# Optimization experiments

Hardware: AMD Instinct MI355X
Metric: run time of the kernel (lower is better)

The kernel has to match this reference:

```python
import jax, jax.numpy as jnp
import numpy as np

NEG_INF = -1e9  # masked_fill value in torch code
HELP_THRESH = -1e8  # help_scores > -1e8 marks valid dependency entries


def setup_inputs() -> dict:
    key = jax.random.key(0)
    ks = jax.random.split(key, 16)
    B, S, D, H, DK = 8, 512, 1024, 16, 64
    sc = 0.02
    x = jax.random.normal(ks[0], (B, S, D), jnp.float32)
    Wq = jax.random.normal(ks[1], (D, H * DK), jnp.float32) * sc
    bq = jax.random.normal(ks[2], (H * DK,), jnp.float32) * sc
    Wk = jax.random.normal(ks[3], (D, H * DK), jnp.float32) * sc
    bk = jax.random.normal(ks[4], (H * DK,), jnp.float32) * sc
    Wv = jax.random.normal(ks[5], (D, H * DK), jnp.float32) * sc
    bv = jax.random.normal(ks[6], (H * DK,), jnp.float32) * sc
    Wo = jax.random.normal(ks[7], (H * DK, D), jnp.float32) * sc
    bo = jax.random.normal(ks[8], (D,), jnp.float32) * sc
    ln_g = jnp.ones((D,), jnp.float32)
    ln_b = jnp.zeros((D,), jnp.float32)
    help_vals = jax.random.normal(ks[9], (B, H, S, S), jnp.float32)
    help_mask = jax.random.randint(ks[10], (B, H, S, S), 0, 2).astype(jnp.int32)
    attn_mask = jax.random.randint(ks[11], (B, S, S), 0, 2).astype(bool)
    return {"x": x, "Wq": Wq, "bq": bq, "Wk": Wk, "bk": bk, "Wv": Wv,
            "bv": bv, "Wo": Wo, "bo": bo, "ln_g": ln_g, "ln_b": ln_b,
            "help_vals": help_vals, "help_mask": help_mask, "attn_mask": attn_mask}


def reference(x, Wq, bq, Wk, bk, Wv, bv, Wo, bo, ln_g, ln_b,
              help_vals, help_mask, attn_mask):
    B, S, D = x.shape
    H, DK = 16, 64
    # projections -> [B,H,S,dk]
    q = (x @ Wq + bq).reshape(B, S, H, DK).transpose(0, 2, 1, 3)
    k = (x @ Wk + bk).reshape(B, S, H, DK).transpose(0, 2, 1, 3)
    v = (x @ Wv + bv).reshape(B, S, H, DK).transpose(0, 2, 1, 3)
    scores = jnp.einsum('bhqd,bhkd->bhqk', q, k) / np.sqrt(DK).astype(np.float32)
    scores = jnp.where(attn_mask[:, None, :, :], NEG_INF, scores)
    # dependency-tree score blending (ScaledDotProductAttention)
    help_scores = jnp.where(help_mask.astype(bool), help_vals, NEG_INF)
    m = (help_scores > HELP_THRESH).astype(scores.dtype)
    dep_w = m * 0.5
    seq_w = m * 0.5 + (1.0 - m)
    scores = help_scores * dep_w + scores * seq_w
    attn = jax.nn.softmax(scores, axis=-1)
    ctx = jnp.einsum('bhqk,bhkd->bhqd', attn, v)  # [B,H,S,dv]
    ctx = ctx.transpose(0, 2, 1, 3).reshape(B, S, H * DK)
    out = ctx @ Wo + bo
    # residual + LayerNorm (input_dim == output_dim path)
    y = out + x
    mu = y.mean(-1, keepdims=True)
    var = ((y - mu) ** 2).mean(-1, keepdims=True)
    y = (y - mu) / jnp.sqrt(var + 1e-5) * ln_g + ln_b
    return y, attn
```

## Files before the change

### kernel.cpp

```cpp
#include <hip/hip_runtime.h>
#include <hip/hip_bf16.h>

typedef __bf16 bf16_t;
typedef __bf16 bf16x4 __attribute__((ext_vector_type(4)));
typedef __bf16 bf16x8 __attribute__((ext_vector_type(8)));
typedef float f32x4 __attribute__((ext_vector_type(4)));
typedef int i32x4 __attribute__((ext_vector_type(4)));


__device__ __forceinline__ f32x4 mfma16(bf16x8 a, bf16x8 b, f32x4 c) {
    return __builtin_amdgcn_mfma_f32_16x16x32_bf16(a, b, c, 0, 0, 0);
}

__device__ __forceinline__ float blendf(float s, int am, int hm, float hv) {
    s = am ? -1e9f : s;
    return hm ? 0.5f * hv + 0.5f * s : s;
}

#define GLOAD_LDS16(g, l)                                                   \
    __builtin_amdgcn_global_load_lds(                                       \
        (const __attribute__((address_space(1))) void*)(g),                 \
        (__attribute__((address_space(3))) void*)(l), 16, 0, 0)

__global__ __launch_bounds__(256) void cast_kernel(const float* __restrict__ x,
                                                   bf16_t* __restrict__ xb) {
    size_t i = ((size_t)blockIdx.x * 256 + threadIdx.x) * 4;
    float4 v = *(const float4*)(x + i);
    bf16x4 o;
    o[0] = (bf16_t)v.x; o[1] = (bf16_t)v.y; o[2] = (bf16_t)v.z; o[3] = (bf16_t)v.w;
    *(bf16x4*)(xb + i) = o;
}

__global__ __launch_bounds__(256) void transpose_kernel(const float* __restrict__ Wq,
                                                        const float* __restrict__ Wk,
                                                        const float* __restrict__ Wv,
                                                        const float* __restrict__ Wo,
                                                        bf16_t* __restrict__ Wt_base) {
    __shared__ float tile[32][33];
    const int z = blockIdx.z;
    const float* W = (z == 0) ? Wq : (z == 1) ? Wk : (z == 2) ? Wv : Wo;
    bf16_t* Wt = Wt_base + ((size_t)z << 20);
    int tx = threadIdx.x & 31, ty = threadIdx.x >> 5;
    int bx = blockIdx.x * 32, by = blockIdx.y * 32;
#pragma unroll
    for (int j = 0; j < 4; j++)
        tile[ty + j * 8][tx] = W[(size_t)(by + ty + j * 8) * 1024 + bx + tx];
    __syncthreads();
#pragma unroll
    for (int j = 0; j < 4; j++)
        Wt[(size_t)(bx + ty + j * 8) * 1024 + by + tx] = (bf16_t)tile[tx][ty + j * 8];
}

__global__ __launch_bounds__(256, 4) void gemm_qkv(const bf16_t* __restrict__ A,
                                                   const bf16_t* __restrict__ WtB,
                                                   const float* __restrict__ bq,
                                                   const float* __restrict__ bk,
                                                   const float* __restrict__ bv,
                                                   bf16_t* __restrict__ qb,
                                                   bf16_t* __restrict__ kb,
                                                   bf16_t* __restrict__ vt) {
    constexpr int K = 1024;
    __shared__ bf16_t As[2][128][32];
    __shared__ bf16_t Bs[2][128][32];
    const int z = blockIdx.z;
    const bf16_t* Bt = WtB + ((size_t)z << 20);
    const float* bias = (z == 0) ? bq : (z == 1) ? bk : bv;
    const int t = threadIdx.x;
    const int lane = t & 63, wv = t >> 6;
    const int lm = lane & 15, q4 = lane >> 4;
    const int mblk = blockIdx.y * 128, nblk = blockIdx.x * 128;
    const int mrow = (wv & 1) * 64, ncol = (wv >> 1) * 64;
    const int sr = t >> 2, sc = (t & 3) * 8;

    f32x4 acc[4][4];
#pragma unroll
    for (int r = 0; r < 4; r++)
#pragma unroll
        for (int c = 0; c < 4; c++) acc[r][c] = (f32x4){0.f, 0.f, 0.f, 0.f};

    const bf16_t* ga = &A[(size_t)(mblk + sr) * K + sc];
    const bf16_t* gb = &Bt[(size_t)(nblk + sr) * K + sc];
    GLOAD_LDS16(ga, &As[0][sr][sc]);
    GLOAD_LDS16(ga + (size_t)64 * K, &As[0][sr + 64][sc]);
    GLOAD_LDS16(gb, &Bs[0][sr][sc]);
    GLOAD_LDS16(gb + (size_t)64 * K, &Bs[0][sr + 64][sc]);
    __syncthreads();

    int cur = 0;
    for (int k0 = 0; k0 < K; k0 += 32) {
        if (k0 + 32 < K) {
            const bf16_t* ga2 = ga + k0 + 32;
            const bf16_t* gb2 = gb + k0 + 32;
            GLOAD_LDS16(ga2, &As[cur ^ 1][sr][sc]);
            GLOAD_LDS16(ga2 + (size_t)64 * K, &As[cur ^ 1][sr + 64][sc]);
            GLOAD_LDS16(gb2, &Bs[cur ^ 1][sr][sc]);
            GLOAD_LDS16(gb2 + (size_t)64 * K, &Bs[cur ^ 1][sr + 64][sc]);
        }
        bf16x8 af[4], bfr[4];
#pragma unroll
        for (int r = 0; r < 4; r++) af[r] = *(const bf16x8*)&As[cur][mrow + r * 16 + lm][q4 * 8];
#pragma unroll
        for (int c = 0; c < 4; c++) bfr[c] = *(const bf16x8*)&Bs[cur][ncol + c * 16 + lm][q4 * 8];
#pragma unroll
        for (int r = 0; r < 4; r++)
#pragma unroll
            for (int c = 0; c < 4; c++) acc[r][c] = mfma16(af[r], bfr[c], acc[r][c]);
        __syncthreads();
        cur ^= 1;
    }

#pragma unroll
    for (int r = 0; r < 4; r++)
#pragma unroll
        for (int c = 0; c < 4; c++)
#pragma unroll
            for (int i = 0; i < 4; i++) {
                int m = mblk + mrow + r * 16 + q4 * 4 + i;
                int n = nblk + ncol + c * 16 + lm;
                float v = acc[r][c][i] + bias[n];
                int b = m >> 9, s = m & 511, h = n >> 6, d = n & 63;
                if (z < 2) {
                    bf16_t* o = z ? kb : qb;
                    o[(((size_t)(b * 16 + h) * 512) + s) * 64 + d] = (bf16_t)v;
                } else {
                    vt[(((size_t)(b * 16 + h) * 64) + d) * 512 + s] = (bf16_t)v;
                }
            }
}

__global__ __launch_bounds__(256, 4) void gemm_out(const bf16_t* __restrict__ A,
                                                   const bf16_t* __restrict__ Bt,
                                                   const float* __restrict__ bias,
                                                   const float* __restrict__ resid,
                                                   float* __restrict__ outp) {
    constexpr int K = 1024, N = 1024;
    __shared__ bf16_t As[2][128][32];
    __shared__ bf16_t Bs[2][128][32];
    const int t = threadIdx.x;
    const int lane = t & 63, wv = t >> 6;
    const int lm = lane & 15, q4 = lane >> 4;
    const int mblk = blockIdx.y * 128, nblk = blockIdx.x * 128;
    const int mrow = (wv & 1) * 64, ncol = (wv >> 1) * 64;
    const int sr = t >> 2, sc = (t & 3) * 8;

    f32x4 acc[4][4];
#pragma unroll
    for (int r = 0; r < 4; r++)
#pragma unroll
        for (int c = 0; c < 4; c++) acc[r][c] = (f32x4){0.f, 0.f, 0.f, 0.f};

    const bf16_t* ga = &A[(size_t)(mblk + sr) * K + sc];
    const bf16_t* gb = &Bt[(size_t)(nblk + sr) * K + sc];
    GLOAD_LDS16(ga, &As[0][sr][sc]);
    GLOAD_LDS16(ga + (size_t)64 * K, &As[0][sr + 64][sc]);
    GLOAD_LDS16(gb, &Bs[0][sr][sc]);
    GLOAD_LDS16(gb + (size_t)64 * K, &Bs[0][sr + 64][sc]);
    __syncthreads();

    int cur = 0;
    for (int k0 = 0; k0 < K; k0 += 32) {
        if (k0 + 32 < K) {
            const bf16_t* ga2 = ga + k0 + 32;
            const bf16_t* gb2 = gb + k0 + 32;
            GLOAD_LDS16(ga2, &As[cur ^ 1][sr][sc]);
            GLOAD_LDS16(ga2 + (size_t)64 * K, &As[cur ^ 1][sr + 64][sc]);
            GLOAD_LDS16(gb2, &Bs[cur ^ 1][sr][sc]);
            GLOAD_LDS16(gb2 + (size_t)64 * K, &Bs[cur ^ 1][sr + 64][sc]);
        }
        bf16x8 af[4], bfr[4];
#pragma unroll
        for (int r = 0; r < 4; r++) af[r] = *(const bf16x8*)&As[cur][mrow + r * 16 + lm][q4 * 8];
#pragma unroll
        for (int c = 0; c < 4; c++) bfr[c] = *(const bf16x8*)&Bs[cur][ncol + c * 16 + lm][q4 * 8];
#pragma unroll
        for (int r = 0; r < 4; r++)
#pragma unroll
            for (int c = 0; c < 4; c++) acc[r][c] = mfma16(af[r], bfr[c], acc[r][c]);
        __syncthreads();
        cur ^= 1;
    }

#pragma unroll
    for (int r = 0; r < 4; r++)
#pragma unroll
        for (int c = 0; c < 4; c++)
#pragma unroll
            for (int i = 0; i < 4; i++) {
                int m = mblk + mrow + r * 16 + q4 * 4 + i;
                int n = nblk + ncol + c * 16 + lm;
                float v = acc[r][c][i] + bias[n];
                outp[(size_t)m * N + n] = v + resid[(size_t)m * N + n];
            }
}

__global__ __launch_bounds__(512, 8) void attn_fused_kernel(const bf16_t* __restrict__ Qb,
                                                            const bf16_t* __restrict__ Kb,
                                                            const bf16_t* __restrict__ Vt,
                                                            const float* __restrict__ help_vals,
                                                            const int* __restrict__ help_mask,
                                                            const int* __restrict__ attn_mask,
                                                            float* __restrict__ attn_out,
                                                            bf16_t* __restrict__ xo) {
    constexpr int SS = 516;
    const int t = threadIdx.x;
    const int lane = t & 63, wv = t >> 6;
    const int lm = lane & 15, q4 = lane >> 4;
    const int bh = blockIdx.y;
    const int b = bh >> 4, h = bh & 15;
    const int q0 = blockIdx.x * 16;
    const bf16_t* Qp = Qb + (size_t)bh * 512 * 64;
    const bf16_t* Kp = Kb + (size_t)bh * 512 * 64;
    const bf16_t* Vp = Vt + (size_t)bh * 64 * 512;

    __shared__ float S[16][SS];
    __shared__ float ctx[16][68];

    for (int i = t; i < 16 * 68; i += 512) ((float*)ctx)[i] = 0.f;

    const bf16x8 bq0 = *(const bf16x8*)&Qp[(size_t)(q0 + lm) * 64 + q4 * 8];
    const bf16x8 bq1 = *(const bf16x8*)&Qp[(size_t)(q0 + lm) * 64 + 32 + q4 * 8];
    f32x4 acc[4];
#pragma unroll
    for (int j = 0; j < 4; j++) acc[j] = (f32x4){0.f, 0.f, 0.f, 0.f};
    __builtin_amdgcn_s_setprio(1);
#pragma unroll
    for (int j = 0; j < 4; j++) {
        const int krow = wv * 64 + j * 16 + lm;
        bf16x8 ak0 = *(const bf16x8*)&Kp[(size_t)krow * 64 + q4 * 8];
        bf16x8 ak1 = *(const bf16x8*)&Kp[(size_t)krow * 64 + 32 + q4 * 8];
        acc[j] = mfma16(ak0, bq0, acc[j]);
        acc[j] = mfma16(ak1, bq1, acc[j]);
    }
    __builtin_amdgcn_s_setprio(0);
#pragma unroll
    for (int j = 0; j < 4; j++)
        *(f32x4*)&S[lm][wv * 64 + j * 16 + q4 * 4] = acc[j] * 0.125f;

    const int c0 = lane * 4, c1 = 256 + lane * 4;
    const int rbase = wv * 2;
    const size_t qrow0 = ((size_t)bh * 512 + q0 + rbase) * 512;
    const size_t arow0 = ((size_t)b * 512 + q0 + rbase) * 512;
    f32x4 hv[2][2];
    i32x4 hm[2][2], am[2][2];
#pragma unroll
    for (int rr = 0; rr < 2; rr++) {
        const size_t qr = qrow0 + (size_t)rr * 512;
        const size_t ar = arow0 + (size_t)rr * 512;
        hv[rr][0] = __builtin_nontemporal_load((const f32x4*)&help_vals[qr + c0]);
        hv[rr][1] = __builtin_nontemporal_load((const f32x4*)&help_vals[qr + c1]);
        hm[rr][0] = __builtin_nontemporal_load((const i32x4*)&help_mask[qr + c0]);
        hm[rr][1] = __builtin_nontemporal_load((const i32x4*)&help_mask[qr + c1]);
        am[rr][0] = *(const i32x4*)&attn_mask[ar + c0];
        am[rr][1] = *(const i32x4*)&attn_mask[ar + c1];
    }
    __builtin_amdgcn_sched_barrier(0);
    __syncthreads();

#pragma unroll
    for (int rr = 0; rr < 2; rr++) {
        const int r = rbase + rr;
        const size_t qrow = qrow0 + (size_t)rr * 512;
        f32x4 s0 = *(const f32x4*)&S[r][c0];
        f32x4 s1 = *(const f32x4*)&S[r][c1];
        float sv[8];
#pragma unroll
        for (int i = 0; i < 4; i++) sv[i] = blendf(s0[i], am[rr][0][i], hm[rr][0][i], hv[rr][0][i]);
#pragma unroll
        for (int i = 0; i < 4; i++)
            sv[4 + i] = blendf(s1[i], am[rr][1][i], hm[rr][1][i], hv[rr][1][i]);
        float mloc = fmaxf(fmaxf(fmaxf(sv[0], sv[1]), fmaxf(sv[2], sv[3])),
                           fmaxf(fmaxf(sv[4], sv[5]), fmaxf(sv[6], sv[7])));
#pragma unroll
        for (int off = 1; off < 64; off <<= 1) mloc = fmaxf(mloc, __shfl_xor(mloc, off));
        float lsum = 0.f;
#pragma unroll
        for (int i = 0; i < 8; i++) {
            sv[i] = __expf(sv[i] - mloc);
            lsum += sv[i];
        }
#pragma unroll
        for (int off = 1; off < 64; off <<= 1) lsum += __shfl_xor(lsum, off);
        const float rinv = 1.0f / lsum;
        f32x4 o0, o1;
        o0[0] = sv[0] * rinv; o0[1] = sv[1] * rinv; o0[2] = sv[2] * rinv; o0[3] = sv[3] * rinv;
        o1[0] = sv[4] * rinv; o1[1] = sv[5] * rinv; o1[2] = sv[6] * rinv; o1[3] = sv[7] * rinv;
        *(f32x4*)&S[r][c0] = o0;
        *(f32x4*)&S[r][c1] = o1;
        __builtin_nontemporal_store(o0, (f32x4*)&attn_out[qrow + c0]);
        __builtin_nontemporal_store(o1, (f32x4*)&attn_out[qrow + c1]);
    }
    __syncthreads();

    f32x4 acc2[4];
#pragma unroll
    for (int mt = 0; mt < 4; mt++) acc2[mt] = (f32x4){0.f, 0.f, 0.f, 0.f};
    const int kb0 = wv * 64;
    __builtin_amdgcn_s_setprio(1);
#pragma unroll
    for (int C = 0; C < 2; C++) {
        f32x4 pa = *(const f32x4*)&S[lm][kb0 + C * 32 + q4 * 8];
        f32x4 pb = *(const f32x4*)&S[lm][kb0 + C * 32 + q4 * 8 + 4];
        bf16x8 pf;
        pf[0] = (bf16_t)pa[0]; pf[1] = (bf16_t)pa[1]; pf[2] = (bf16_t)pa[2]; pf[3] = (bf16_t)pa[3];
        pf[4] = (bf16_t)pb[0]; pf[5] = (bf16_t)pb[1]; pf[6] = (bf16_t)pb[2]; pf[7] = (bf16_t)pb[3];
#pragma unroll
        for (int mt = 0; mt < 4; mt++) {
            const bf16x8 vf =
                *(const bf16x8*)&Vp[(size_t)(mt * 16 + lm) * 512 + kb0 + C * 32 + q4 * 8];
            acc2[mt] = mfma16(vf, pf, acc2[mt]);
        }
    }
    __builtin_amdgcn_s_setprio(0);
#pragma unroll
    for (int mt = 0; mt < 4; mt++)
#pragma unroll
        for (int i = 0; i < 4; i++) atomicAdd(&ctx[lm][mt * 16 + q4 * 4 + i], acc2[mt][i]);
    __syncthreads();

    if (t < 256) {
        const int qq = t >> 4;
        const int d4 = (t & 15) * 4;
        f32x4 sum = *(const f32x4*)&ctx[qq][d4];
        bf16x4 o;
        o[0] = (bf16_t)sum[0]; o[1] = (bf16_t)sum[1];
        o[2] = (bf16_t)sum[2]; o[3] = (bf16_t)sum[3];
        *(bf16x4*)&xo[((size_t)(b * 512 + q0 + qq)) * 1024 + h * 64 + d4] = o;
    }
}

__global__ __launch_bounds__(256) void layernorm_kernel(const float* __restrict__ ypre,
                                                        const float* __restrict__ g,
                                                        const float* __restrict__ bvec,
                                                        float* __restrict__ out) {
    int row = blockIdx.x;
    int t = threadIdx.x;
    float4 v = ((const float4*)(ypre + (size_t)row * 1024))[t];
    float s = v.x + v.y + v.z + v.w;
    float sq = v.x * v.x + v.y * v.y + v.z * v.z + v.w * v.w;
#pragma unroll
    for (int off = 32; off; off >>= 1) {
        s += __shfl_down(s, off);
        sq += __shfl_down(sq, off);
    }
    __shared__ float ss[4], ssq[4];
    if ((t & 63) == 0) { ss[t >> 6] = s; ssq[t >> 6] = sq; }
    __syncthreads();
    float tot = ss[0] + ss[1] + ss[2] + ss[3];
    float totq = ssq[0] + ssq[1] + ssq[2] + ssq[3];
    float mu = tot * (1.0f / 1024.0f);
    float var = totq * (1.0f / 1024.0f) - mu * mu;
    float rstd = rsqrtf(var + 1e-5f);
    float4 gg = ((const float4*)g)[t];
    float4 bb = ((const float4*)bvec)[t];
    float4 o;
    o.x = (v.x - mu) * rstd * gg.x + bb.x;
    o.y = (v.y - mu) * rstd * gg.y + bb.y;
    o.z = (v.z - mu) * rstd * gg.z + bb.z;
    o.w = (v.w - mu) * rstd * gg.w + bb.w;
    ((float4*)(out + (size_t)row * 1024))[t] = o;
}

extern "C" void kernel_launch(void* const* d_in, const int* in_sizes, int n_in,
                              void* d_out, int out_size, void* d_ws, size_t ws_size,
                              hipStream_t stream) {
    const float* x         = (const float*)d_in[0];
    const float* Wq        = (const float*)d_in[1];
    const float* bq        = (const float*)d_in[2];
    const float* Wk        = (const float*)d_in[3];
    const float* bk        = (const float*)d_in[4];
    const float* Wv        = (const float*)d_in[5];
    const float* bv        = (const float*)d_in[6];
    const float* Wo        = (const float*)d_in[7];
    const float* bo        = (const float*)d_in[8];
    const float* ln_g      = (const float*)d_in[9];
    const float* ln_b      = (const float*)d_in[10];
    const float* help_vals = (const float*)d_in[11];
    const int*   help_mask = (const int*)d_in[12];
    const int*   attn_mask = (const int*)d_in[13];

    char* ws = (char*)d_ws;
    bf16_t* xb   = (bf16_t*)(ws);
    bf16_t* wqt  = (bf16_t*)(ws + ((size_t)8 << 20));
    bf16_t* wot  = (bf16_t*)(ws + ((size_t)14 << 20));
    bf16_t* qb   = (bf16_t*)(ws + ((size_t)16 << 20));
    bf16_t* kb   = (bf16_t*)(ws + ((size_t)24 << 20));
    bf16_t* vt   = (bf16_t*)(ws + ((size_t)32 << 20));
    bf16_t* xo   = (bf16_t*)(ws + ((size_t)40 << 20));
    float*  ypre = (float*)(ws + ((size_t)48 << 20));

    float* y_out = (float*)d_out;
    float* attn_out = y_out + (size_t)4096 * 1024;

    cast_kernel<<<4096, 256, 0, stream>>>(x, xb);
    transpose_kernel<<<dim3(32, 32, 4), 256, 0, stream>>>(Wq, Wk, Wv, Wo, wqt);

    gemm_qkv<<<dim3(8, 32, 3), 256, 0, stream>>>(xb, wqt, bq, bk, bv, qb, kb, vt);

    attn_fused_kernel<<<dim3(32, 128), 512, 0, stream>>>(qb, kb, vt, help_vals, help_mask,
                                                         attn_mask, attn_out, xo);

    gemm_out<<<dim3(8, 32), 256, 0, stream>>>(xo, wot, bo, x, ypre);
    layernorm_kernel<<<4096, 256, 0, stream>>>(ypre, ln_g, ln_b, y_out);
}
```

Before: 579.0 us.

## Make attention kernel persistent over eight tiles with prefetched help/mask streams

The attention kernel now launches 512 blocks, and each block loops over 8 consecutive (bh, q-tile) tiles instead of handling one tile per block. While the current tile is being processed, the help_vals, help_mask and attn_mask loads for the next tile are issued after softmax, so the memory traffic overlaps with the PV MFMA work. The intent is to hide global load latency and cut block launch overhead. In exchange it adds extra barriers and a ctx reset per tile, and drops the occupancy hint from 8 to 4, which could leave less parallelism to hide latency.

```diff
diff --git a/kernel.cpp b/kernel.cpp
--- a/kernel.cpp
+++ b/kernel.cpp
@@ -193,7 +193,7 @@
             }
 }
 
-__global__ __launch_bounds__(512, 8) void attn_fused_kernel(const bf16_t* __restrict__ Qb,
+__global__ __launch_bounds__(512, 4) void attn_fused_kernel(const bf16_t* __restrict__ Qb,
                                                             const bf16_t* __restrict__ Kb,
                                                             const bf16_t* __restrict__ Vt,
                                                             const float* __restrict__ help_vals,
@@ -205,127 +205,153 @@
     const int t = threadIdx.x;
     const int lane = t & 63, wv = t >> 6;
     const int lm = lane & 15, q4 = lane >> 4;
-    const int bh = blockIdx.y;
-    const int b = bh >> 4, h = bh & 15;
-    const int q0 = blockIdx.x * 16;
-    const bf16_t* Qp = Qb + (size_t)bh * 512 * 64;
-    const bf16_t* Kp = Kb + (size_t)bh * 512 * 64;
-    const bf16_t* Vp = Vt + (size_t)bh * 64 * 512;
 
     __shared__ float S[16][SS];
     __shared__ float ctx[16][68];
 
     for (int i = t; i < 16 * 68; i += 512) ((float*)ctx)[i] = 0.f;
 
-    const bf16x8 bq0 = *(const bf16x8*)&Qp[(size_t)(q0 + lm) * 64 + q4 * 8];
-    const bf16x8 bq1 = *(const bf16x8*)&Qp[(size_t)(q0 + lm) * 64 + 32 + q4 * 8];
-    f32x4 acc[4];
-#pragma unroll
-    for (int j = 0; j < 4; j++) acc[j] = (f32x4){0.f, 0.f, 0.f, 0.f};
-    __builtin_amdgcn_s_setprio(1);
-#pragma unroll
-    for (int j = 0; j < 4; j++) {
-        const int krow = wv * 64 + j * 16 + lm;
-        bf16x8 ak0 = *(const bf16x8*)&Kp[(size_t)krow * 64 + q4 * 8];
-        bf16x8 ak1 = *(const bf16x8*)&Kp[(size_t)krow * 64 + 32 + q4 * 8];
-        acc[j] = mfma16(ak0, bq0, acc[j]);
-        acc[j] = mfma16(ak1, bq1, acc[j]);
-    }
-    __builtin_amdgcn_s_setprio(0);
-#pragma unroll
-    for (int j = 0; j < 4; j++)
-        *(f32x4*)&S[lm][wv * 64 + j * 16 + q4 * 4] = acc[j] * 0.125f;
-
     const int c0 = lane * 4, c1 = 256 + lane * 4;
     const int rbase = wv * 2;
-    const size_t qrow0 = ((size_t)bh * 512 + q0 + rbase) * 512;
-    const size_t arow0 = ((size_t)b * 512 + q0 + rbase) * 512;
+
     f32x4 hv[2][2];
     i32x4 hm[2][2], am[2][2];
-#pragma unroll
-    for (int rr = 0; rr < 2; rr++) {
-        const size_t qr = qrow0 + (size_t)rr * 512;
-        const size_t ar = arow0 + (size_t)rr * 512;
-        hv[rr][0] = __builtin_nontemporal_load((const f32x4*)&help_vals[qr + c0]);
-        hv[rr][1] = __builtin_nontemporal_load((const f32x4*)&help_vals[qr + c1]);
-        hm[rr][0] = __builtin_nontemporal_load((const i32x4*)&help_mask[qr + c0]);
-        hm[rr][1] = __builtin_nontemporal_load((const i32x4*)&help_mask[qr + c1]);
-        am[rr][0] = *(const i32x4*)&attn_mask[ar + c0];
-        am[rr][1] = *(const i32x4*)&attn_mask[ar + c1];
+
+#define ISSUE_STREAMS(TID)                                                              \
+    do {                                                                                \
+        const int bh_ = (TID) >> 5;                                                     \
+        const int q0_ = ((TID) & 31) << 4;                                              \
+        const size_t qr0_ = ((size_t)bh_ * 512 + q0_ + rbase) * 512;                    \
+        const size_t ar0_ = ((size_t)(bh_ >> 4) * 512 + q0_ + rbase) * 512;             \
+        _Pragma("unroll") for (int rr = 0; rr < 2; rr++) {                              \
+            const size_t qr_ = qr0_ + (size_t)rr * 512;                                 \
+            const size_t ar_ = ar0_ + (size_t)rr * 512;                                 \
+            hv[rr][0] = __builtin_nontemporal_load((const f32x4*)&help_vals[qr_ + c0]); \
+            hv[rr][1] = __builtin_nontemporal_load((const f32x4*)&help_vals[qr_ + c1]); \
+            hm[rr][0] = __builtin_nontemporal_load((const i32x4*)&help_mask[qr_ + c0]); \
+            hm[rr][1] = __builtin_nontemporal_load((const i32x4*)&help_mask[qr_ + c1]); \
+            am[rr][0] = *(const i32x4*)&attn_mask[ar_ + c0];                            \
+            am[rr][1] = *(const i32x4*)&attn_mask[ar_ + c1];                            \
+        }                                                                               \
+    } while (0)
+
+    int tid = blockIdx.x * 8;
+    ISSUE_STREAMS(tid);
+    __builtin_amdgcn_sched_barrier(0);
+
+    for (int it = 0; it < 8; ++it, ++tid) {
+        const int bh = tid >> 5;
+        const int b = bh >> 4, h = bh & 15;
+        const int q0 = (tid & 31) << 4;
+        const bf16_t* Qp = Qb + (size_t)bh * 512 * 64;
+        const bf16_t* Kp = Kb + (size_t)bh * 512 * 64;
+        const bf16_t* Vp = Vt + (size_t)bh * 64 * 512;
+        const size_t qrow0 = ((size_t)bh * 512 + q0 + rbase) * 512;
+
+        const bf16x8 bq0 = *(const bf16x8*)&Qp[(size_t)(q0 + lm) * 64 + q4 * 8];
+        const bf16x8 bq1 = *(const bf16x8*)&Qp[(size_t)(q0 + lm) * 64 + 32 + q4 * 8];
+        f32x4 acc[4];
+#pragma unroll
+        for (int j = 0; j < 4; j++) acc[j] = (f32x4){0.f, 0.f, 0.f, 0.f};
+        __builtin_amdgcn_s_setprio(1);
+#pragma unroll
+        for (int j = 0; j < 4; j++) {
+            const int krow = wv * 64 + j * 16 + lm;
+            bf16x8 ak0 = *(const bf16x8*)&Kp[(size_t)krow * 64 + q4 * 8];
+            bf16x8 ak1 = *(const bf16x8*)&Kp[(size_t)krow * 64 + 32 + q4 * 8];
+            acc[j] = mfma16(ak0, bq0, acc[j]);
+            acc[j] = mfma16(ak1, bq1, acc[j]);
+        }
+        __builtin_amdgcn_s_setprio(0);
+#pragma unroll
+        for (int j = 0; j < 4; j++)
+            *(f32x4*)&S[lm][wv * 64 + j * 16 + q4 * 4] = acc[j] * 0.125f;
+        __syncthreads();
+
+#pragma unroll
+        for (int rr = 0; rr < 2; rr++) {
+            const int r = rbase + rr;
+            const size_t qrow = qrow0 + (size_t)rr * 512;
+            f32x4 s0 = *(const f32x4*)&S[r][c0];
+            f32x4 s1 = *(const f32x4*)&S[r][c1];
+            float sv[8];
+#pragma unroll
+            for (int i = 0; i < 4; i++)
+                sv[i] = blendf(s0[i], am[rr][0][i], hm[rr][0][i], hv[rr][0][i]);
+#pragma unroll
+            for (int i = 0; i < 4; i++)
+                sv[4 + i] = blendf(s1[i], am[rr][1][i], hm[rr][1][i], hv[rr][1][i]);
+            float mloc = fmaxf(fmaxf(fmaxf(sv[0], sv[1]), fmaxf(sv[2], sv[3])),
+                               fmaxf(fmaxf(sv[4], sv[5]), fmaxf(sv[6], sv[7])));
+#pragma unroll
+            for (int off = 1; off < 64; off <<= 1) mloc = fmaxf(mloc, __shfl_xor(mloc, off));
+            float lsum = 0.f;
+#pragma unroll
+            for (int i = 0; i < 8; i++) {
+                sv[i] = __expf(sv[i] - mloc);
+                lsum += sv[i];
+            }
+#pragma unroll
+            for (int off = 1; off < 64; off <<= 1) lsum += __shfl_xor(lsum, off);
+            const float rinv = 1.0f / lsum;
+            f32x4 o0, o1;
+            o0[0] = sv[0] * rinv; o0[1] = sv[1] * rinv;
+            o0[2] = sv[2] * rinv; o0[3] = sv[3] * rinv;
+            o1[0] = sv[4] * rinv; o1[1] = sv[5] * rinv;
+            o1[2] = sv[6] * rinv; o1[3] = sv[7] * rinv;
+            *(f32x4*)&S[r][c0] = o0;
+            *(f32x4*)&S[r][c1] = o1;
+            __builtin_nontemporal_store(o0, (f32x4*)&attn_out[qrow + c0]);
+            __builtin_nontemporal_store(o1, (f32x4*)&attn_out[qrow + c1]);
+        }
+        if (it < 7) {
+            ISSUE_STREAMS(tid + 1);
+            __builtin_amdgcn_sched_barrier(0);
+        }
+        __syncthreads();
+
+        f32x4 acc2[4];
+#pragma unroll
+        for (int mt = 0; mt < 4; mt++) acc2[mt] = (f32x4){0.f, 0.f, 0.f, 0.f};
+        const int kb0 = wv * 64;
+        __builtin_amdgcn_s_setprio(1);
+#pragma unroll
+        for (int C = 0; C < 2; C++) {
+            f32x4 pa = *(const f32x4*)&S[lm][kb0 + C * 32 + q4 * 8];
+            f32x4 pb = *(const f32x4*)&S[lm][kb0 + C * 32 + q4 * 8 + 4];
+            bf16x8 pf;
+            pf[0] = (bf16_t)pa[0]; pf[1] = (bf16_t)pa[1];
+            pf[2] = (bf16_t)pa[2]; pf[3] = (bf16_t)pa[3];
+            pf[4] = (bf16_t)pb[0]; pf[5] = (bf16_t)pb[1];
+            pf[6] = (bf16_t)pb[2]; pf[7] = (bf16_t)pb[3];
+#pragma unroll
+            for (int mt = 0; mt < 4; mt++) {
+                const bf16x8 vf =
+                    *(const bf16x8*)&Vp[(size_t)(mt * 16 + lm) * 512 + kb0 + C * 32 + q4 * 8];
+                acc2[mt] = mfma16(vf, pf, acc2[mt]);
+            }
+        }
+        __builtin_amdgcn_s_setprio(0);
+#pragma unroll
+        for (int mt = 0; mt < 4; mt++)
+#pragma unroll
+            for (int i = 0; i < 4; i++) atomicAdd(&ctx[lm][mt * 16 + q4 * 4 + i], acc2[mt][i]);
+        __syncthreads();
+
+        if (t < 256) {
+            const int qq = t >> 4;
+            const int d4 = (t & 15) * 4;
+            f32x4 sum = *(const f32x4*)&ctx[qq][d4];
+            bf16x4 o;
+            o[0] = (bf16_t)sum[0]; o[1] = (bf16_t)sum[1];
+            o[2] = (bf16_t)sum[2]; o[3] = (bf16_t)sum[3];
+            *(bf16x4*)&xo[((size_t)(b * 512 + q0 + qq)) * 1024 + h * 64 + d4] = o;
+        }
+        __syncthreads();
+        if (it < 7)
+            for (int i = t; i < 16 * 68; i += 512) ((float*)ctx)[i] = 0.f;
     }
-    __builtin_amdgcn_sched_barrier(0);
-    __syncthreads();
-
-#pragma unroll
-    for (int rr = 0; rr < 2; rr++) {
-        const int r = rbase + rr;
-        const size_t qrow = qrow0 + (size_t)rr * 512;
-        f32x4 s0 = *(const f32x4*)&S[r][c0];
-        f32x4 s1 = *(const f32x4*)&S[r][c1];
-        float sv[8];
-#pragma unroll
-        for (int i = 0; i < 4; i++) sv[i] = blendf(s0[i], am[rr][0][i], hm[rr][0][i], hv[rr][0][i]);
-#pragma unroll
-        for (int i = 0; i < 4; i++)
-            sv[4 + i] = blendf(s1[i], am[rr][1][i], hm[rr][1][i], hv[rr][1][i]);
-        float mloc = fmaxf(fmaxf(fmaxf(sv[0], sv[1]), fmaxf(sv[2], sv[3])),
-                           fmaxf(fmaxf(sv[4], sv[5]), fmaxf(sv[6], sv[7])));
-#pragma unroll
-        for (int off = 1; off < 64; off <<= 1) mloc = fmaxf(mloc, __shfl_xor(mloc, off));
-        float lsum = 0.f;
-#pragma unroll
-        for (int i = 0; i < 8; i++) {
-            sv[i] = __expf(sv[i] - mloc);
-            lsum += sv[i];
-        }
-#pragma unroll
-        for (int off = 1; off < 64; off <<= 1) lsum += __shfl_xor(lsum, off);
-        const float rinv = 1.0f / lsum;
-        f32x4 o0, o1;
-        o0[0] = sv[0] * rinv; o0[1] = sv[1] * rinv; o0[2] = sv[2] * rinv; o0[3] = sv[3] * rinv;
-        o1[0] = sv[4] * rinv; o1[1] = sv[5] * rinv; o1[2] = sv[6] * rinv; o1[3] = sv[7] * rinv;
-        *(f32x4*)&S[r][c0] = o0;
-        *(f32x4*)&S[r][c1] = o1;
-        __builtin_nontemporal_store(o0, (f32x4*)&attn_out[qrow + c0]);
-        __builtin_nontemporal_store(o1, (f32x4*)&attn_out[qrow + c1]);
-    }
-    __syncthreads();
-
-    f32x4 acc2[4];
-#pragma unroll
-    for (int mt = 0; mt < 4; mt++) acc2[mt] = (f32x4){0.f, 0.f, 0.f, 0.f};
-    const int kb0 = wv * 64;
-    __builtin_amdgcn_s_setprio(1);
-#pragma unroll
-    for (int C = 0; C < 2; C++) {
-        f32x4 pa = *(const f32x4*)&S[lm][kb0 + C * 32 + q4 * 8];
-        f32x4 pb = *(const f32x4*)&S[lm][kb0 + C * 32 + q4 * 8 + 4];
-        bf16x8 pf;
-        pf[0] = (bf16_t)pa[0]; pf[1] = (bf16_t)pa[1]; pf[2] = (bf16_t)pa[2]; pf[3] = (bf16_t)pa[3];
-        pf[4] = (bf16_t)pb[0]; pf[5] = (bf16_t)pb[1]; pf[6] = (bf16_t)pb[2]; pf[7] = (bf16_t)pb[3];
-#pragma unroll
-        for (int mt = 0; mt < 4; mt++) {
-            const bf16x8 vf =
-                *(const bf16x8*)&Vp[(size_t)(mt * 16 + lm) * 512 + kb0 + C * 32 + q4 * 8];
-            acc2[mt] = mfma16(vf, pf, acc2[mt]);
-        }
-    }
-    __builtin_amdgcn_s_setprio(0);
-#pragma unroll
-    for (int mt = 0; mt < 4; mt++)
-#pragma unroll
-        for (int i = 0; i < 4; i++) atomicAdd(&ctx[lm][mt * 16 + q4 * 4 + i], acc2[mt][i]);
-    __syncthreads();
-
-    if (t < 256) {
-        const int qq = t >> 4;
-        const int d4 = (t & 15) * 4;
-        f32x4 sum = *(const f32x4*)&ctx[qq][d4];
-        bf16x4 o;
-        o[0] = (bf16_t)sum[0]; o[1] = (bf16_t)sum[1];
-        o[2] = (bf16_t)sum[2]; o[3] = (bf16_t)sum[3];
-        *(bf16x4*)&xo[((size_t)(b * 512 + q0 + qq)) * 1024 + h * 64 + d4] = o;
-    }
+#undef ISSUE_STREAMS
 }
 
 __global__ __launch_bounds__(256) void layernorm_kernel(const float* __restrict__ ypre,
@@ -396,8 +422,8 @@
 
     gemm_qkv<<<dim3(8, 32, 3), 256, 0, stream>>>(xb, wqt, bq, bk, bv, qb, kb, vt);
 
-    attn_fused_kernel<<<dim3(32, 128), 512, 0, stream>>>(qb, kb, vt, help_vals, help_mask,
-                                                         attn_mask, attn_out, xo);
+    attn_fused_kernel<<<512, 512, 0, stream>>>(qb, kb, vt, help_vals, help_mask,
+                                               attn_mask, attn_out, xo);
 
     gemm_out<<<dim3(8, 32), 256, 0, stream>>>(xo, wot, bo, x, ypre);
     layernorm_kernel<<<4096, 256, 0, stream>>>(ypre, ln_g, ln_b, y_out);
```

Measured after the change: 621.2 us. 7.3% more time.
